# Kernel optimization log

Measured on AMD Instinct MI355X. Metric: run time of the kernel, lower is better.

Reference implementation:

```python
import jax, jax.numpy as jnp
import numpy as np

IMAGE_SIZE = 288.0
LAMBDA_NOOBJ = 0.5
LAMBDA_COOR = 5.0
_ANCHOR_DIMS = np.array([[0.24, 0.24], [0.12, 0.12], [0.08, 0.08], [0.28, 0.28], [0.15, 0.15]], np.float32)
ANCHORS = jnp.concatenate([jnp.full((5, 2), 0.5, jnp.float32), jnp.asarray(_ANCHOR_DIMS)], axis=1)  # [cx,cy,w,h]


def _corners(box):
    # matches torch _format_bbox column order used in _get_iou: (x1, x2, y1, y2)
    cx, cy, w, h = box[..., 0], box[..., 1], box[..., 2], box[..., 3]
    return cx - w / 2, cx + w / 2, cy - h / 2, cy + h / 2


def _iou(b1, b2):
    x1a, x2a, y1a, y2a = _corners(b1)
    x1b, x2b, y1b, y2b = _corners(b2)
    iw = jnp.minimum(x2a, x2b) - jnp.maximum(x1a, x1b) + 1.0
    ih = jnp.minimum(y2a, y2b) - jnp.maximum(y1a, y1b) + 1.0
    inter = iw * ih
    a1 = (x2a - x1a + 1.0) * (y2a - y1a + 1.0)
    a2 = (x2b - x1b + 1.0) * (y2b - y1b + 1.0)
    return inter / (a1 + a2 - inter + 1e-16)


def setup_inputs() -> dict:
    key = jax.random.key(0)
    k1, k2, k3, k4 = jax.random.split(key, 4)
    B, G, A, T = 32, 36, 5, 8
    return {
        "bbox_prediction": jax.random.normal(k1, (B, G, G, A, 5), jnp.float32),
        "landmarks_prediction": jax.random.normal(k2, (B, G, G, A, 68, 2), jnp.float32),
        "bbox_target": jax.random.uniform(k3, (B, T, 4), jnp.float32),
        "landmarks_target": jax.random.uniform(k4, (B, T, 68, 2), jnp.float32),
    }


def _forward(bbox_prediction, landmarks_prediction, bbox_target, landmarks_target):
    B, G, _, A, _ = bbox_prediction.shape
    T = bbox_target.shape[1]
    N = B * G * G * A

    valid = bbox_target.sum(-1) != 0  # (B,T)
    gx = bbox_target[..., 0] * G
    gy = bbox_target[..., 1] * G
    gi = jnp.floor(gx).astype(jnp.int32)  # int(gt_x)
    gj = jnp.floor(gy).astype(jnp.int32)
    fx = gx - gi
    fy = gy - gj
    gt_anchor_box = jnp.stack([fx, fy, bbox_target[..., 2], bbox_target[..., 3]], -1)  # (B,T,4)

    # vectorized anchor assignment (replaces per-target python loop)
    anchor_iou = _iou(gt_anchor_box[:, :, None, :], ANCHORS[None, None, :, :])  # (B,T,A)
    best_a = jnp.argmax(anchor_iou, -1).astype(jnp.int32)
    log_box = jnp.log1p(gt_anchor_box)  # (B,T,4) -- torch stores log1p form

    lin = ((jnp.arange(B)[:, None] * G + gj) * G + gi) * A + best_a  # (B,T) flat (b,j,i,a)
    lin = jnp.where(valid, lin, N)  # invalid targets -> dump slot N

    obj = jnp.zeros(N + 1, jnp.float32).at[lin.ravel()].set(1.0)[:N].reshape(B, G, G, A)
    noobj = 1.0 - obj

    t_ids = jnp.broadcast_to(jnp.arange(T, dtype=jnp.int32), (B, T))
    seg_last = jax.ops.segment_max(t_ids.ravel(), lin.ravel(), num_segments=N + 1)
    winner = (seg_last[lin] == t_ids) & valid
    lin_w = jnp.where(winner, lin, N).ravel()

    gt_boxes = jnp.zeros((N + 1, 4), jnp.float32).at[lin_w].set(log_box.reshape(-1, 4))[:N].reshape(B, G, G, A, 4)
    gt_lm = jnp.zeros((N + 1, 136), jnp.float32).at[lin_w].set(landmarks_target.reshape(B * T, 136))[:N].reshape(B, G, G, A, 136)

    nobj = jnp.maximum(obj.sum(), 1.0)

    # NME over object cells (masked-mean expressed as weighted sum -> static shapes)
    diff = landmarks_prediction.reshape(B, G, G, A, 136) - gt_lm
    dist = jnp.sqrt(jnp.sum(diff * diff, -1))  # (B,G,G,A)
    wh = gt_boxes[..., 2] * gt_boxes[..., 3]  # note: log1p(w)*log1p(h), as in torch
    norm = jnp.sqrt(jnp.where(obj > 0, wh, 1.0)) * IMAGE_SIZE * 68.0 * nobj
    nme = jnp.sum(obj * dist / norm)

    # localization: SmoothL1 (beta=1), mean over masked elements
    d = bbox_prediction[..., :4] - gt_boxes
    ad = jnp.abs(d)
    sl1 = jnp.where(ad < 1.0, 0.5 * d * d, ad - 0.5)
    loc_loss = LAMBDA_COOR * jnp.sum(obj[..., None] * sl1) / (nobj * 4.0)

    # confidence: MSE on noobj (target 0) + MSE on obj (target 1)
    conf_pred = bbox_prediction[..., 4]
    n_noobj = jnp.maximum(noobj.sum(), 1.0)
    conf_loss = LAMBDA_NOOBJ * jnp.sum(noobj * conf_pred ** 2) / n_noobj + jnp.sum(obj * (conf_pred - 1.0) ** 2) / nobj

    # best predicted bbox per target (IoU of log1p gt box vs raw cell predictions, as in torch)
    cell_pred = bbox_prediction[jnp.arange(B)[:, None], gj, gi]  # (B,T,A,5)
    pred_iou = _iou(log_box[:, :, None, :], cell_pred[..., :4])  # (B,T,A)
    best_p = jnp.argmax(pred_iou, -1)
    best = jnp.take_along_axis(cell_pred, best_p[..., None, None], axis=2)[:, :, 0]  # (B,T,5)
    x1, x2, y1, y2 = _corners(best[..., :4])
    best_pred = jnp.where(valid[..., None], jnp.stack([x1, x2, y1, y2, best[..., 4]], -1), 0.0)

    return nme, loc_loss, conf_loss, best_pred


def reference(bbox_prediction, landmarks_prediction, bbox_target, landmarks_target):
    return _forward(bbox_prediction, landmarks_prediction, bbox_target, landmarks_target)
```

## Files before the change

### kernel.cpp

```cpp
#include <hip/hip_runtime.h>
#include <math.h>

#define Gc 36
#define Ac 5
#define Bc 32
#define Tc 8
#define NCELLS (Bc*Gc*Gc*Ac)
#define NFLOATS (NCELLS*5)
#define NF4 (NFLOATS/4)
#define NT 256
#define CONF_BLOCKS 128


__device__ __forceinline__ void target_meta(const float* __restrict__ bbox_tgt,
                                            int tgt, bool& valid, int& gi, int& gj,
                                            float& fx, float& fy, float& w, float& h,
                                            int& best_a) {
    const float* tg = bbox_tgt + (size_t)tgt * 4;
    float x = tg[0], y = tg[1];
    w = tg[2]; h = tg[3];
    valid = ((x + y + w + h) != 0.0f);
    float gx = x * (float)Gc, gy = y * (float)Gc;
    gi = (int)floorf(gx); gj = (int)floorf(gy);
    fx = gx - floorf(gx); fy = gy - floorf(gy);

    float x1a = fx - w * 0.5f, x2a = fx + w * 0.5f;
    float y1a = fy - h * 0.5f, y2a = fy + h * 0.5f;
    float a1 = (x2a - x1a + 1.0f) * (y2a - y1a + 1.0f);
    const float adim[Ac] = {0.24f, 0.12f, 0.08f, 0.28f, 0.15f};
    best_a = 0;
    float best_iou = -1e30f;
    for (int a = 0; a < Ac; ++a) {
        float x1b = 0.5f - adim[a] * 0.5f, x2b = 0.5f + adim[a] * 0.5f;
        float iw = fminf(x2a, x2b) - fmaxf(x1a, x1b) + 1.0f;
        float ih = fminf(y2a, x2b) - fmaxf(y1a, x1b) + 1.0f;
        float inter = iw * ih;
        float a2 = (x2b - x1b + 1.0f) * (x2b - x1b + 1.0f);
        float iou = inter / (a1 + a2 - inter + 1e-16f);
        if (iou > best_iou) { best_iou = iou; best_a = a; }
    }
}

__global__ __launch_bounds__(NT) void k12_conf_lm(
        const float* __restrict__ bbox_pred,
        const float* __restrict__ lm_pred,
        const float* __restrict__ bbox_tgt,
        const float* __restrict__ lm_tgt,
        float* __restrict__ ws_f, int* __restrict__ ws_i) {
    if (blockIdx.x < CONF_BLOCKS) {
        __shared__ float red[NT];
        const float4* p4 = (const float4*)bbox_pred;
        float acc = 0.0f;
        for (int j = blockIdx.x * NT + threadIdx.x; j < NF4;
             j += CONF_BLOCKS * NT) {
            float4 f = p4[j];
            int r = (4 * j) % 5;
            float v = (r == 4) ? f.x : (r == 3) ? f.y : (r == 2) ? f.z
                    : (r == 1) ? f.w : 0.0f;
            acc += v * v;
        }
        red[threadIdx.x] = acc;
        __syncthreads();
        for (int s = NT / 2; s > 0; s >>= 1) {
            if (threadIdx.x < s) red[threadIdx.x] += red[threadIdx.x + s];
            __syncthreads();
        }
        if (threadIdx.x == 0) ws_f[blockIdx.x] = red[0];
    } else {
        const int tgt = blockIdx.x - CONF_BLOCKS;
        const int b = tgt >> 3, t = tgt & 7;
        const int tid = threadIdx.x;
        __shared__ int s_lin8[8];

        if (tid < 8) {
            bool v; int gi, gj, ba; float fx, fy, w, h;
            target_meta(bbox_tgt, (b << 3) + tid, v, gi, gj, fx, fy, w, h, ba);
            s_lin8[tid] = v ? (((b * Gc + gj) * Gc + gi) * Ac + ba) : NCELLS;
        }
        __syncthreads();

        if (tid < 64) {
            int lin = s_lin8[t];
            bool valid = (lin != NCELLS);
            bool winner = valid;
            if (valid)
                for (int t2 = t + 1; t2 < Tc; ++t2)
                    if (s_lin8[t2] == lin) { winner = false; break; }

            float acc = 0.0f;
            if (winner && tid < 34) {
                const float4* lp = (const float4*)(lm_pred + (size_t)lin * 136);
                const float4* lt = (const float4*)(lm_tgt + (size_t)tgt * 136);
                float4 a = lp[tid], c = lt[tid];
                float dx = a.x - c.x, dy = a.y - c.y;
                float dz = a.z - c.z, dw = a.w - c.w;
                acc = dx * dx + dy * dy + dz * dz + dw * dw;
            }
            for (int off = 32; off > 0; off >>= 1)
                acc += __shfl_down(acc, off, 64);

            if (tid == 0) {
                ws_i[256 + tgt] = lin;
                ws_i[512 + tgt] = winner ? 1 : 0;
                ws_f[1024 + tgt] = winner ? sqrtf(acc) : 0.0f;
            }
        }
    }
}

__device__ __forceinline__ float block_sum(float v, float* red, int tid) {
    red[tid] = v;
    __syncthreads();
    for (int s = NT / 2; s > 0; s >>= 1) {
        if (tid < s) red[tid] += red[tid + s];
        __syncthreads();
    }
    float r = red[0];
    __syncthreads();
    return r;
}

__global__ __launch_bounds__(NT) void k3_final(
        const float* __restrict__ bbox_pred,
        const float* __restrict__ bbox_tgt,
        const float* __restrict__ ws_f,
        const int* __restrict__ ws_i,
        float* __restrict__ out) {
    const int tid = threadIdx.x;
    const int b = tid >> 3;
    __shared__ float s_red[NT];
    __shared__ int s_cnt[NT];

    bool valid; int gi, gj, best_a; float fx, fy, w, h;
    target_meta(bbox_tgt, tid, valid, gi, gj, fx, fy, w, h, best_a);
    int lin = ws_i[256 + tid];
    int winner = ws_i[512 + tid];
    float dist = ws_f[1024 + tid];

    float l0 = log1pf(fx), l1 = log1pf(fy), l2 = log1pf(w), l3 = log1pf(h);

    float c_nme = 0.0f, c_sl1 = 0.0f, c_cobj = 0.0f, c_csq = 0.0f;
    if (winner) {
        const float* bp = bbox_pred + (size_t)lin * 5;
        float conf = bp[4];
        c_cobj = (conf - 1.0f) * (conf - 1.0f);
        c_csq = conf * conf;
        float lb[4] = {l0, l1, l2, l3};
        for (int k = 0; k < 4; ++k) {
            float d = bp[k] - lb[k];
            float ad = fabsf(d);
            c_sl1 += (ad < 1.0f) ? 0.5f * d * d : (ad - 0.5f);
        }
        c_nme = dist / (sqrtf(l2 * l3) * 288.0f * 68.0f);
    }

    s_cnt[tid] = winner;
    __syncthreads();
    for (int s = NT / 2; s > 0; s >>= 1) {
        if (tid < s) s_cnt[tid] += s_cnt[tid + s];
        __syncthreads();
    }
    int cnt = s_cnt[0];
    __syncthreads();
    float nobj = fmaxf((float)cnt, 1.0f);
    float n_noobj = fmaxf((float)(NCELLS - cnt), 1.0f);

    float sum_nme  = block_sum(c_nme, s_red, tid);
    float sum_sl1  = block_sum(c_sl1, s_red, tid);
    float sum_cobj = block_sum(c_cobj, s_red, tid);
    float sum_csq  = block_sum(c_csq, s_red, tid);
    float s_total  = block_sum(tid < CONF_BLOCKS ? ws_f[tid] : 0.0f, s_red, tid);

    if (tid == 0) {
        out[0] = sum_nme / nobj;
        out[1] = 5.0f * sum_sl1 / (nobj * 4.0f);
        out[2] = 0.5f * (s_total - sum_csq) / n_noobj + sum_cobj / nobj;
    }

    const float* cp = bbox_pred + (size_t)((b * Gc + gj) * Gc + gi) * Ac * 5;
    float x1g = l0 - l2 * 0.5f, x2g = l0 + l2 * 0.5f;
    float y1g = l1 - l3 * 0.5f, y2g = l1 + l3 * 0.5f;
    float ag = (x2g - x1g + 1.0f) * (y2g - y1g + 1.0f);
    int bp_idx = 0;
    float bp_iou = -1e30f;
    for (int a = 0; a < Ac; ++a) {
        float cx = cp[a * 5 + 0], cy = cp[a * 5 + 1];
        float pw = cp[a * 5 + 2], ph = cp[a * 5 + 3];
        float x1p = cx - pw * 0.5f, x2p = cx + pw * 0.5f;
        float y1p = cy - ph * 0.5f, y2p = cy + ph * 0.5f;
        float iw = fminf(x2g, x2p) - fmaxf(x1g, x1p) + 1.0f;
        float ih = fminf(y2g, y2p) - fmaxf(y1g, y1p) + 1.0f;
        float inter = iw * ih;
        float ap = (x2p - x1p + 1.0f) * (y2p - y1p + 1.0f);
        float iou = inter / (ag + ap - inter + 1e-16f);
        if (iou > bp_iou) { bp_iou = iou; bp_idx = a; }
    }
    float bx = cp[bp_idx * 5 + 0], by = cp[bp_idx * 5 + 1];
    float bw = cp[bp_idx * 5 + 2], bh = cp[bp_idx * 5 + 3];
    float bconf = cp[bp_idx * 5 + 4];
    float* op = out + 3 + (size_t)tid * 5;
    if (valid) {
        op[0] = bx - bw * 0.5f; op[1] = bx + bw * 0.5f;
        op[2] = by - bh * 0.5f; op[3] = by + bh * 0.5f; op[4] = bconf;
    } else {
        op[0] = 0.0f; op[1] = 0.0f; op[2] = 0.0f; op[3] = 0.0f; op[4] = 0.0f;
    }
}

extern "C" void kernel_launch(void* const* d_in, const int* in_sizes, int n_in,
                              void* d_out, int out_size, void* d_ws, size_t ws_size,
                              hipStream_t stream) {
    const float* bbox_pred = (const float*)d_in[0];
    const float* lm_pred   = (const float*)d_in[1];
    const float* bbox_tgt  = (const float*)d_in[2];
    const float* lm_tgt    = (const float*)d_in[3];
    float* out = (float*)d_out;
    float* ws_f = (float*)d_ws;
    int* ws_i = (int*)d_ws;

    k12_conf_lm<<<CONF_BLOCKS + 256, NT, 0, stream>>>(bbox_pred, lm_pred,
                                                      bbox_tgt, lm_tgt,
                                                      ws_f, ws_i);
    k3_final<<<1, NT, 0, stream>>>(bbox_pred, bbox_tgt, ws_f, ws_i, out);
}
```

Measured before the change: 157.8 us.

## Fuse two kernels into one cooperative launch with grid sync

Merges the partial-reduction/landmark kernel and the single-block finalization kernel into one cooperative kernel, using a grid-wide barrier between phases, with a fallback to the two-launch path if the cooperative launch fails. The final block's five sequential block reductions are also folded into one combined tree reduction over a float4, a scalar and a count. This aims to remove a kernel launch gap and cut barrier count in the final step. It adds grid-sync overhead and the cooperative launch path's extra cost.

```diff
diff --git a/kernel.cpp b/kernel.cpp
--- a/kernel.cpp
+++ b/kernel.cpp
@@ -1,5 +1,8 @@
 #include <hip/hip_runtime.h>
+#include <hip/hip_cooperative_groups.h>
 #include <math.h>
+
+namespace cg = cooperative_groups;
 
 #define Gc 36
 #define Ac 5
@@ -41,95 +44,83 @@
     }
 }
 
-__global__ __launch_bounds__(NT) void k12_conf_lm(
-        const float* __restrict__ bbox_pred,
-        const float* __restrict__ lm_pred,
-        const float* __restrict__ bbox_tgt,
-        const float* __restrict__ lm_tgt,
-        float* __restrict__ ws_f, int* __restrict__ ws_i) {
-    if (blockIdx.x < CONF_BLOCKS) {
-        __shared__ float red[NT];
-        const float4* p4 = (const float4*)bbox_pred;
-        float acc = 0.0f;
-        for (int j = blockIdx.x * NT + threadIdx.x; j < NF4;
-             j += CONF_BLOCKS * NT) {
-            float4 f = p4[j];
-            int r = (4 * j) % 5;
-            float v = (r == 4) ? f.x : (r == 3) ? f.y : (r == 2) ? f.z
-                    : (r == 1) ? f.w : 0.0f;
-            acc += v * v;
-        }
-        red[threadIdx.x] = acc;
-        __syncthreads();
-        for (int s = NT / 2; s > 0; s >>= 1) {
-            if (threadIdx.x < s) red[threadIdx.x] += red[threadIdx.x + s];
-            __syncthreads();
-        }
-        if (threadIdx.x == 0) ws_f[blockIdx.x] = red[0];
-    } else {
-        const int tgt = blockIdx.x - CONF_BLOCKS;
-        const int b = tgt >> 3, t = tgt & 7;
-        const int tid = threadIdx.x;
-        __shared__ int s_lin8[8];
-
-        if (tid < 8) {
-            bool v; int gi, gj, ba; float fx, fy, w, h;
-            target_meta(bbox_tgt, (b << 3) + tid, v, gi, gj, fx, fy, w, h, ba);
-            s_lin8[tid] = v ? (((b * Gc + gj) * Gc + gi) * Ac + ba) : NCELLS;
-        }
-        __syncthreads();
-
-        if (tid < 64) {
-            int lin = s_lin8[t];
-            bool valid = (lin != NCELLS);
-            bool winner = valid;
-            if (valid)
-                for (int t2 = t + 1; t2 < Tc; ++t2)
-                    if (s_lin8[t2] == lin) { winner = false; break; }
-
-            float acc = 0.0f;
-            if (winner && tid < 34) {
-                const float4* lp = (const float4*)(lm_pred + (size_t)lin * 136);
-                const float4* lt = (const float4*)(lm_tgt + (size_t)tgt * 136);
-                float4 a = lp[tid], c = lt[tid];
-                float dx = a.x - c.x, dy = a.y - c.y;
-                float dz = a.z - c.z, dw = a.w - c.w;
-                acc = dx * dx + dy * dy + dz * dz + dw * dw;
-            }
-            for (int off = 32; off > 0; off >>= 1)
-                acc += __shfl_down(acc, off, 64);
-
-            if (tid == 0) {
-                ws_i[256 + tgt] = lin;
-                ws_i[512 + tgt] = winner ? 1 : 0;
-                ws_f[1024 + tgt] = winner ? sqrtf(acc) : 0.0f;
-            }
-        }
-    }
-}
-
-__device__ __forceinline__ float block_sum(float v, float* red, int tid) {
-    red[tid] = v;
+__device__ __forceinline__ void do_conf(const float* __restrict__ bbox_pred,
+                                        float* __restrict__ ws_f) {
+    __shared__ float red[NT];
+    const float4* p4 = (const float4*)bbox_pred;
+    float acc = 0.0f;
+    for (int j = blockIdx.x * NT + threadIdx.x; j < NF4;
+         j += CONF_BLOCKS * NT) {
+        float4 f = p4[j];
+        int r = (4 * j) % 5;
+        float v = (r == 4) ? f.x : (r == 3) ? f.y : (r == 2) ? f.z
+                : (r == 1) ? f.w : 0.0f;
+        acc += v * v;
+    }
+    red[threadIdx.x] = acc;
     __syncthreads();
     for (int s = NT / 2; s > 0; s >>= 1) {
-        if (tid < s) red[tid] += red[tid + s];
+        if (threadIdx.x < s) red[threadIdx.x] += red[threadIdx.x + s];
         __syncthreads();
     }
-    float r = red[0];
+    if (threadIdx.x == 0) ws_f[blockIdx.x] = red[0];
+}
+
+__device__ __forceinline__ void do_target(const float* __restrict__ lm_pred,
+                                          const float* __restrict__ bbox_tgt,
+                                          const float* __restrict__ lm_tgt,
+                                          float* __restrict__ ws_f,
+                                          int* __restrict__ ws_i) {
+    const int tgt = blockIdx.x - CONF_BLOCKS;
+    const int b = tgt >> 3, t = tgt & 7;
+    const int tid = threadIdx.x;
+    __shared__ int s_lin8[8];
+
+    if (tid < 8) {
+        bool v; int gi, gj, ba; float fx, fy, w, h;
+        target_meta(bbox_tgt, (b << 3) + tid, v, gi, gj, fx, fy, w, h, ba);
+        s_lin8[tid] = v ? (((b * Gc + gj) * Gc + gi) * Ac + ba) : NCELLS;
+    }
     __syncthreads();
-    return r;
-}
-
-__global__ __launch_bounds__(NT) void k3_final(
-        const float* __restrict__ bbox_pred,
-        const float* __restrict__ bbox_tgt,
-        const float* __restrict__ ws_f,
-        const int* __restrict__ ws_i,
-        float* __restrict__ out) {
+
+    if (tid < 64) {
+        int lin = s_lin8[t];
+        bool valid = (lin != NCELLS);
+        bool winner = valid;
+        if (valid)
+            for (int t2 = t + 1; t2 < Tc; ++t2)
+                if (s_lin8[t2] == lin) { winner = false; break; }
+
+        float acc = 0.0f;
+        if (winner && tid < 34) {
+            const float4* lp = (const float4*)(lm_pred + (size_t)lin * 136);
+            const float4* lt = (const float4*)(lm_tgt + (size_t)tgt * 136);
+            float4 a = lp[tid], c = lt[tid];
+            float dx = a.x - c.x, dy = a.y - c.y;
+            float dz = a.z - c.z, dw = a.w - c.w;
+            acc = dx * dx + dy * dy + dz * dz + dw * dw;
+        }
+        for (int off = 32; off > 0; off >>= 1)
+            acc += __shfl_down(acc, off, 64);
+
+        if (tid == 0) {
+            ws_i[256 + tgt] = lin;
+            ws_i[512 + tgt] = winner ? 1 : 0;
+            ws_f[1024 + tgt] = winner ? sqrtf(acc) : 0.0f;
+        }
+    }
+}
+
+__device__ __forceinline__ void do_final(const float* __restrict__ bbox_pred,
+                                         const float* __restrict__ bbox_tgt,
+                                         const float* __restrict__ ws_f,
+                                         const int* __restrict__ ws_i,
+                                         float* __restrict__ out) {
     const int tid = threadIdx.x;
     const int b = tid >> 3;
-    __shared__ float s_red[NT];
-    __shared__ int s_cnt[NT];
+    __shared__ float4 s_red4[NT];
+    __shared__ float  s_reds[NT];
+    __shared__ int    s_cnt[NT];
 
     bool valid; int gi, gj, best_a; float fx, fy, w, h;
     target_meta(bbox_tgt, tid, valid, gi, gj, fx, fy, w, h, best_a);
@@ -155,26 +146,29 @@
     }
 
     s_cnt[tid] = winner;
+    s_red4[tid] = make_float4(c_nme, c_sl1, c_cobj, c_csq);
+    s_reds[tid] = (tid < CONF_BLOCKS) ? ws_f[tid] : 0.0f;
     __syncthreads();
     for (int s = NT / 2; s > 0; s >>= 1) {
-        if (tid < s) s_cnt[tid] += s_cnt[tid + s];
+        if (tid < s) {
+            s_cnt[tid] += s_cnt[tid + s];
+            float4 a = s_red4[tid], c = s_red4[tid + s];
+            a.x += c.x; a.y += c.y; a.z += c.z; a.w += c.w;
+            s_red4[tid] = a;
+            s_reds[tid] += s_reds[tid + s];
+        }
         __syncthreads();
     }
-    int cnt = s_cnt[0];
-    __syncthreads();
-    float nobj = fmaxf((float)cnt, 1.0f);
-    float n_noobj = fmaxf((float)(NCELLS - cnt), 1.0f);
-
-    float sum_nme  = block_sum(c_nme, s_red, tid);
-    float sum_sl1  = block_sum(c_sl1, s_red, tid);
-    float sum_cobj = block_sum(c_cobj, s_red, tid);
-    float sum_csq  = block_sum(c_csq, s_red, tid);
-    float s_total  = block_sum(tid < CONF_BLOCKS ? ws_f[tid] : 0.0f, s_red, tid);
 
     if (tid == 0) {
-        out[0] = sum_nme / nobj;
-        out[1] = 5.0f * sum_sl1 / (nobj * 4.0f);
-        out[2] = 0.5f * (s_total - sum_csq) / n_noobj + sum_cobj / nobj;
+        int cnt = s_cnt[0];
+        float nobj = fmaxf((float)cnt, 1.0f);
+        float n_noobj = fmaxf((float)(NCELLS - cnt), 1.0f);
+        float4 sums = s_red4[0];
+        float s_total = s_reds[0];
+        out[0] = sums.x / nobj;
+        out[1] = 5.0f * sums.y / (nobj * 4.0f);
+        out[2] = 0.5f * (s_total - sums.w) / n_noobj + sums.z / nobj;
     }
 
     const float* cp = bbox_pred + (size_t)((b * Gc + gj) * Gc + gi) * Ac * 5;
@@ -207,6 +201,46 @@
     }
 }
 
+__global__ __launch_bounds__(NT) void k_fused(
+        const float* __restrict__ bbox_pred,
+        const float* __restrict__ lm_pred,
+        const float* __restrict__ bbox_tgt,
+        const float* __restrict__ lm_tgt,
+        float* __restrict__ ws_f, int* __restrict__ ws_i,
+        float* __restrict__ out) {
+    if (blockIdx.x < CONF_BLOCKS) {
+        do_conf(bbox_pred, ws_f);
+    } else {
+        do_target(lm_pred, bbox_tgt, lm_tgt, ws_f, ws_i);
+    }
+    cg::this_grid().sync();
+    if (blockIdx.x == 0) {
+        do_final(bbox_pred, bbox_tgt, ws_f, ws_i, out);
+    }
+}
+
+__global__ __launch_bounds__(NT) void k12_conf_lm(
+        const float* __restrict__ bbox_pred,
+        const float* __restrict__ lm_pred,
+        const float* __restrict__ bbox_tgt,
+        const float* __restrict__ lm_tgt,
+        float* __restrict__ ws_f, int* __restrict__ ws_i) {
+    if (blockIdx.x < CONF_BLOCKS) {
+        do_conf(bbox_pred, ws_f);
+    } else {
+        do_target(lm_pred, bbox_tgt, lm_tgt, ws_f, ws_i);
+    }
+}
+
+__global__ __launch_bounds__(NT) void k3_final(
+        const float* __restrict__ bbox_pred,
+        const float* __restrict__ bbox_tgt,
+        const float* __restrict__ ws_f,
+        const int* __restrict__ ws_i,
+        float* __restrict__ out) {
+    do_final(bbox_pred, bbox_tgt, ws_f, ws_i, out);
+}
+
 extern "C" void kernel_launch(void* const* d_in, const int* in_sizes, int n_in,
                               void* d_out, int out_size, void* d_ws, size_t ws_size,
                               hipStream_t stream) {
@@ -218,8 +252,14 @@
     float* ws_f = (float*)d_ws;
     int* ws_i = (int*)d_ws;
 
-    k12_conf_lm<<<CONF_BLOCKS + 256, NT, 0, stream>>>(bbox_pred, lm_pred,
-                                                      bbox_tgt, lm_tgt,
-                                                      ws_f, ws_i);
-    k3_final<<<1, NT, 0, stream>>>(bbox_pred, bbox_tgt, ws_f, ws_i, out);
-}
+    void* args[] = {(void*)&bbox_pred, (void*)&lm_pred, (void*)&bbox_tgt,
+                    (void*)&lm_tgt, (void*)&ws_f, (void*)&ws_i, (void*)&out};
+    hipError_t err = hipLaunchCooperativeKernel(
+        (const void*)k_fused, dim3(CONF_BLOCKS + 256), dim3(NT), args, 0, stream);
+    if (err != hipSuccess) {
+        k12_conf_lm<<<CONF_BLOCKS + 256, NT, 0, stream>>>(bbox_pred, lm_pred,
+                                                          bbox_tgt, lm_tgt,
+                                                          ws_f, ws_i);
+        k3_final<<<1, NT, 0, stream>>>(bbox_pred, bbox_tgt, ws_f, ws_i, out);
+    }
+}
```

After: 203.3 us. +28.9%, slower.
